# Optimization experiments

Hardware: AMD Instinct MI355X
Metric: run time of the kernel (lower is better)

## Reference

```python
import jax, jax.numpy as jnp
import numpy as np

HIDDEN = 256


def setup_inputs() -> dict:
    key = jax.random.key(0)
    ks = jax.random.split(key, 6)
    b, c_len, q_len, h = 32, 1024, 128, HIDDEN
    # Xavier-uniform bounds for the learned weights
    lim_vec = float(np.sqrt(6.0 / (h + 1)))      # (h, 1) weights
    lim_cq = float(np.sqrt(6.0 / (1 + h)))       # (1, 1, h) weight
    return {
        "context": jax.random.normal(ks[0], (b, c_len, h), dtype=jnp.float32),
        "query": jax.random.normal(ks[1], (b, q_len, h), dtype=jnp.float32),
        "c_mask": jnp.zeros((b, c_len), dtype=bool),
        "q_mask": jnp.zeros((b, q_len), dtype=bool),
        "c_weight": jax.random.uniform(ks[2], (h, 1), jnp.float32, -lim_vec, lim_vec),
        "q_weight": jax.random.uniform(ks[3], (h, 1), jnp.float32, -lim_vec, lim_vec),
        "cq_weight": jax.random.uniform(ks[4], (1, 1, h), jnp.float32, -lim_cq, lim_cq),
        "bias": jnp.zeros((1,), dtype=jnp.float32),
    }


def reference(context, query, c_mask, q_mask, c_weight, q_weight, cq_weight, bias):
    # Trilinear similarity: S[b,i,j] = c_i.w_c + q_j.w_q + (c_i * w_cq).q_j + bias
    s0 = context @ c_weight                                  # (b, c, 1)
    s1 = jnp.swapaxes(query @ q_weight, 1, 2)                # (b, 1, q)
    s2 = jnp.einsum('bch,bqh->bcq', context * cq_weight, query)
    S = s0 + s1 + s2 + bias                                  # (b, c, q)

    S_bar = jax.nn.softmax(S, axis=1)       # softmax over context axis
    S_bar_bar = jax.nn.softmax(S, axis=2)   # softmax over query axis

    A = jnp.einsum('bcq,bqh->bch', S, query)  # note: raw S, as in source
    B = jnp.einsum('bcq,bkq,bkh->bch', S_bar, S_bar_bar, context)

    return jnp.concatenate([context, A, context * A, context * B], axis=2)
```

## Files before the change

kernel.cpp:

```cpp
#include <hip/hip_runtime.h>
#include <cstdint>
#include <cstddef>

#define BATCH 32
#define CLEN  1024
#define QLEN  128
#define HID   256

typedef __attribute__((ext_vector_type(8))) short bf16x8;
typedef __attribute__((ext_vector_type(4))) float f32x4;

#define MFMA(a, b, c) __builtin_amdgcn_mfma_f32_16x16x32_bf16((a), (b), (c), 0, 0, 0)

__device__ __forceinline__ ushort f2b(float f) {
    union { float f; uint u; } v; v.f = f;
    uint r = (v.u + 0x7fffu + ((v.u >> 16) & 1u)) >> 16;
    return (ushort)r;
}
__device__ __forceinline__ float b2f(ushort u) {
    union { uint u; float f; } v; v.u = ((uint)u) << 16;
    return v.f;
}

__global__ __launch_bounds__(256) void prep_ctx_kernel(
    const float* __restrict__ context, const float* __restrict__ cw,
    ushort* __restrict__ ctxT, float* __restrict__ cdot)
{
    __shared__ ushort lds[64][258];
    int bid = blockIdx.x;
    int b = bid >> 4, c0 = (bid & 15) * 64;
    int t = threadIdx.x;
    int r = t >> 2, qd = t & 3;
    const float* src = context + ((size_t)(b * CLEN + c0 + r)) * HID;
    float dot = 0.f;
    #pragma unroll
    for (int j = 0; j < 16; j++) {
        int h = j * 16 + qd * 4;
        float4 v = *reinterpret_cast<const float4*>(src + h);
        float4 w = *reinterpret_cast<const float4*>(cw + h);
        dot += v.x * w.x + v.y * w.y + v.z * w.z + v.w * w.w;
        uint p0 = (uint)f2b(v.x) | ((uint)f2b(v.y) << 16);
        uint p1 = (uint)f2b(v.z) | ((uint)f2b(v.w) << 16);
        *reinterpret_cast<uint*>(&lds[r][h])     = p0;
        *reinterpret_cast<uint*>(&lds[r][h + 2]) = p1;
    }
    dot += __shfl_xor(dot, 1);
    dot += __shfl_xor(dot, 2);
    if (qd == 0) cdot[b * CLEN + c0 + r] = dot;
    __syncthreads();
    ushort* dst = ctxT + ((size_t)(b * HID + t)) * CLEN + c0;
    #pragma unroll
    for (int j = 0; j < 8; j++) {
        uint4 w;
        w.x = (uint)lds[j*8+0][t] | ((uint)lds[j*8+1][t] << 16);
        w.y = (uint)lds[j*8+2][t] | ((uint)lds[j*8+3][t] << 16);
        w.z = (uint)lds[j*8+4][t] | ((uint)lds[j*8+5][t] << 16);
        w.w = (uint)lds[j*8+6][t] | ((uint)lds[j*8+7][t] << 16);
        *reinterpret_cast<uint4*>(dst + j * 8) = w;
    }
}

__global__ __launch_bounds__(256) void prep_q_kernel(
    const float* __restrict__ query, const float* __restrict__ qw,
    ushort* __restrict__ qB, ushort* __restrict__ qT, float* __restrict__ qdot)
{
    __shared__ ushort lds[64][258];
    int bid = blockIdx.x;
    int b = bid >> 1, q0 = (bid & 1) * 64;
    int t = threadIdx.x;
    int r = t >> 2, qd = t & 3;
    const float* src = query + ((size_t)(b * QLEN + q0 + r)) * HID;
    ushort* qBr = qB + ((size_t)(b * QLEN + q0 + r)) * HID;
    float dot = 0.f;
    #pragma unroll
    for (int j = 0; j < 16; j++) {
        int h = j * 16 + qd * 4;
        float4 v = *reinterpret_cast<const float4*>(src + h);
        float4 w = *reinterpret_cast<const float4*>(qw + h);
        dot += v.x * w.x + v.y * w.y + v.z * w.z + v.w * w.w;
        uint p0 = (uint)f2b(v.x) | ((uint)f2b(v.y) << 16);
        uint p1 = (uint)f2b(v.z) | ((uint)f2b(v.w) << 16);
        *reinterpret_cast<uint*>(&lds[r][h])     = p0;
        *reinterpret_cast<uint*>(&lds[r][h + 2]) = p1;
        uint2 pk; pk.x = p0; pk.y = p1;
        *reinterpret_cast<uint2*>(qBr + h) = pk;
    }
    dot += __shfl_xor(dot, 1);
    dot += __shfl_xor(dot, 2);
    if (qd == 0) qdot[b * QLEN + q0 + r] = dot;
    __syncthreads();
    ushort* dst = qT + ((size_t)(b * HID + t)) * QLEN + q0;
    #pragma unroll
    for (int j = 0; j < 8; j++) {
        uint4 w;
        w.x = (uint)lds[j*8+0][t] | ((uint)lds[j*8+1][t] << 16);
        w.y = (uint)lds[j*8+2][t] | ((uint)lds[j*8+3][t] << 16);
        w.z = (uint)lds[j*8+4][t] | ((uint)lds[j*8+5][t] << 16);
        w.w = (uint)lds[j*8+6][t] | ((uint)lds[j*8+7][t] << 16);
        *reinterpret_cast<uint4*>(dst + j * 8) = w;
    }
}

__global__ __launch_bounds__(256) void s_kernel(
    const float* __restrict__ context, const ushort* __restrict__ qB,
    const float* __restrict__ cqw, const float* __restrict__ cdot,
    const float* __restrict__ qdot, const float* __restrict__ bias,
    ushort* __restrict__ S, ushort* __restrict__ P2T)
{
    __shared__ float ldsS[64][132];
    __shared__ float ldsM[64], ldsR[64];
    int ct = blockIdx.x, b = blockIdx.y;
    int c0 = ct * 64;
    int t = threadIdx.x;
    int w = t >> 6, L = t & 63, g = L >> 4, ln = L & 15;
    int wr = w >> 1, wc = w & 1;

    f32x4 acc[2][4];
    #pragma unroll
    for (int mi = 0; mi < 2; mi++)
        #pragma unroll
        for (int ni = 0; ni < 4; ni++) acc[mi][ni] = (f32x4){0.f, 0.f, 0.f, 0.f};

    const float* ctxB = context + ((size_t)(b * CLEN + c0 + wr * 32)) * HID;
    const ushort* qBb = qB + ((size_t)(b * QLEN + wc * 64)) * HID;

    #pragma unroll 2
    for (int kk = 0; kk < 8; kk++) {
        int k = kk * 32 + g * 8;
        float4 w0 = *reinterpret_cast<const float4*>(cqw + k);
        float4 w1 = *reinterpret_cast<const float4*>(cqw + k + 4);
        bf16x8 a[2];
        #pragma unroll
        for (int mi = 0; mi < 2; mi++) {
            const float* p = ctxB + (size_t)(mi * 16 + ln) * HID + k;
            float4 v0 = *reinterpret_cast<const float4*>(p);
            float4 v1 = *reinterpret_cast<const float4*>(p + 4);
            bf16x8 av;
            av[0] = (short)f2b(v0.x * w0.x); av[1] = (short)f2b(v0.y * w0.y);
            av[2] = (short)f2b(v0.z * w0.z); av[3] = (short)f2b(v0.w * w0.w);
            av[4] = (short)f2b(v1.x * w1.x); av[5] = (short)f2b(v1.y * w1.y);
            av[6] = (short)f2b(v1.z * w1.z); av[7] = (short)f2b(v1.w * w1.w);
            a[mi] = av;
        }
        bf16x8 bq[4];
        #pragma unroll
        for (int ni = 0; ni < 4; ni++)
            bq[ni] = *reinterpret_cast<const bf16x8*>(qBb + (size_t)(ni * 16 + ln) * HID + k);
        #pragma unroll
        for (int mi = 0; mi < 2; mi++)
            #pragma unroll
            for (int ni = 0; ni < 4; ni++)
                acc[mi][ni] = MFMA(a[mi], bq[ni], acc[mi][ni]);
    }

    float bv = bias[0];
    float qdv[4];
    #pragma unroll
    for (int ni = 0; ni < 4; ni++) qdv[ni] = qdot[b * QLEN + wc * 64 + ni * 16 + ln];
    #pragma unroll
    for (int mi = 0; mi < 2; mi++)
        #pragma unroll
        for (int r = 0; r < 4; r++) {
            int row = wr * 32 + mi * 16 + g * 4 + r;
            float cd = cdot[b * CLEN + c0 + row] + bv;
            #pragma unroll
            for (int ni = 0; ni < 4; ni++)
                ldsS[row][wc * 64 + ni * 16 + ln] = acc[mi][ni][r] + cd + qdv[ni];
        }
    __syncthreads();
    {
        int row = t >> 2, qs = (t & 3) * 32;
        float4 vr[8];
        float m = -1e30f;
        #pragma unroll
        for (int j = 0; j < 8; j++) {
            vr[j] = *reinterpret_cast<const float4*>(&ldsS[row][qs + j * 4]);
            m = fmaxf(m, fmaxf(fmaxf(vr[j].x, vr[j].y), fmaxf(vr[j].z, vr[j].w)));
        }
        m = fmaxf(m, __shfl_xor(m, 1));
        m = fmaxf(m, __shfl_xor(m, 2));
        float s = 0.f;
        #pragma unroll
        for (int j = 0; j < 8; j++)
            s += __expf(vr[j].x - m) + __expf(vr[j].y - m) +
                 __expf(vr[j].z - m) + __expf(vr[j].w - m);
        s += __shfl_xor(s, 1);
        s += __shfl_xor(s, 2);
        if ((t & 3) == 0) { ldsM[row] = m; ldsR[row] = 1.0f / s; }
    }
    __syncthreads();
    {
        const size_t Sbase = ((size_t)b * CLEN + c0) * QLEN;
        #pragma unroll
        for (int i = 0; i < 8; i++) {
            int flat = t + 256 * i;
            int q4 = flat & 31, c = flat >> 5;
            float4 v = *reinterpret_cast<const float4*>(&ldsS[c][q4 * 4]);
            uint2 pk;
            pk.x = (uint)f2b(v.x) | ((uint)f2b(v.y) << 16);
            pk.y = (uint)f2b(v.z) | ((uint)f2b(v.w) << 16);
            *reinterpret_cast<uint2*>(&S[Sbase + (size_t)c * QLEN + q4 * 4]) = pk;
        }
    }
    {
        int q = t >> 1, half = t & 1;
        ushort* dst = P2T + ((size_t)b * QLEN + q) * CLEN + c0 + half * 32;
        #pragma unroll
        for (int jo = 0; jo < 4; jo++) {
            uint pk[4];
            #pragma unroll
            for (int l = 0; l < 4; l++) {
                int c0l = half * 32 + jo * 8 + l * 2;
                float p0 = __expf(ldsS[c0l][q]     - ldsM[c0l])     * ldsR[c0l];
                float p1 = __expf(ldsS[c0l + 1][q] - ldsM[c0l + 1]) * ldsR[c0l + 1];
                pk[l] = (uint)f2b(p0) | ((uint)f2b(p1) << 16);
            }
            uint4 wv; wv.x = pk[0]; wv.y = pk[1]; wv.z = pk[2]; wv.w = pk[3];
            *reinterpret_cast<uint4*>(dst + jo * 8) = wv;
        }
    }
}

__global__ __launch_bounds__(256) void colstats1_kernel(
    const ushort* __restrict__ S, float* __restrict__ pmax, float* __restrict__ psum)
{
    int b = blockIdx.x, chunk = blockIdx.y;
    int t = threadIdx.x;
    int q = t & 127, half = t >> 7;
    const ushort* Sb = S + ((size_t)b * CLEN + chunk * 128) * QLEN;
    float m = -1e30f, s = 0.f;
    for (int k = 0; k < 64; k++) {
        int c = half + 2 * k;
        float v = b2f(Sb[(size_t)c * QLEN + q]);
        float nm = fmaxf(m, v);
        s = s * __expf(m - nm) + __expf(v - nm);
        m = nm;
    }
    __shared__ float sm[256], ss[256];
    sm[t] = m; ss[t] = s;
    __syncthreads();
    if (t < 128) {
        float m2 = sm[t + 128], s2 = ss[t + 128];
        float M = fmaxf(m, m2);
        float Sv = s * __expf(m - M) + s2 * __expf(m2 - M);
        pmax[((size_t)b * 8 + chunk) * QLEN + q] = M;
        psum[((size_t)b * 8 + chunk) * QLEN + q] = Sv;
    }
}

__global__ __launch_bounds__(256) void colstats2_kernel(
    const float* __restrict__ pmax, const float* __restrict__ psum,
    float* __restrict__ colmax, float* __restrict__ colsumr)
{
    int gid = blockIdx.x * 256 + threadIdx.x;
    int b = gid >> 7, q = gid & 127;
    float m = -1e30f, s = 0.f;
    #pragma unroll
    for (int ch = 0; ch < 8; ch++) {
        float m2 = pmax[((size_t)b * 8 + ch) * QLEN + q];
        float s2 = psum[((size_t)b * 8 + ch) * QLEN + q];
        float M = fmaxf(m, m2);
        s = s * __expf(m - M) + s2 * __expf(m2 - M);
        m = M;
    }
    colmax[gid] = m;
    colsumr[gid] = 1.0f / s;
}

__global__ __launch_bounds__(256) void t_kernel(
    const ushort* __restrict__ ctxT, const ushort* __restrict__ P2T,
    float* __restrict__ Tpart)
{
    int x = blockIdx.x, b = blockIdx.y;
    int h0 = (x >> 2) * 64, ks = x & 3;
    int t = threadIdx.x;
    int w = t >> 6, L = t & 63, g = L >> 4, ln = L & 15;
    int wr = w >> 1, wc = w & 1;

    f32x4 acc[2][4];
    #pragma unroll
    for (int mi = 0; mi < 2; mi++)
        #pragma unroll
        for (int ni = 0; ni < 4; ni++) acc[mi][ni] = (f32x4){0.f, 0.f, 0.f, 0.f};

    const ushort* aB = ctxT + ((size_t)(b * HID + h0 + wr * 32)) * CLEN + ks * 256;
    const ushort* bB = P2T + ((size_t)(b * QLEN + wc * 64)) * CLEN + ks * 256;

    #pragma unroll 2
    for (int kk = 0; kk < 8; kk++) {
        int k = kk * 32 + g * 8;
        bf16x8 a[2], bq[4];
        #pragma unroll
        for (int mi = 0; mi < 2; mi++)
            a[mi] = *reinterpret_cast<const bf16x8*>(aB + (size_t)(mi * 16 + ln) * CLEN + k);
        #pragma unroll
        for (int ni = 0; ni < 4; ni++)
            bq[ni] = *reinterpret_cast<const bf16x8*>(bB + (size_t)(ni * 16 + ln) * CLEN + k);
        #pragma unroll
        for (int mi = 0; mi < 2; mi++)
            #pragma unroll
            for (int ni = 0; ni < 4; ni++)
                acc[mi][ni] = MFMA(a[mi], bq[ni], acc[mi][ni]);
    }
    float* dst = Tpart + (size_t)ks * (BATCH * HID * QLEN);
    #pragma unroll
    for (int mi = 0; mi < 2; mi++)
        #pragma unroll
        for (int ni = 0; ni < 4; ni++)
            #pragma unroll
            for (int r = 0; r < 4; r++) {
                int h = h0 + wr * 32 + mi * 16 + g * 4 + r;
                int q = wc * 64 + ni * 16 + ln;
                dst[((size_t)b * HID + h) * QLEN + q] = acc[mi][ni][r];
            }
}

__global__ __launch_bounds__(256) void t_reduce_kernel(
    const float* __restrict__ Tpart, ushort* __restrict__ Tt)
{
    int gid = blockIdx.x * 256 + threadIdx.x;
    const float4* p = reinterpret_cast<const float4*>(Tpart);
    float4 a = p[gid];
    float4 b = p[gid + 262144];
    float4 c = p[gid + 524288];
    float4 d = p[gid + 786432];
    float4 r = make_float4(a.x + b.x + c.x + d.x, a.y + b.y + c.y + d.y,
                           a.z + b.z + c.z + d.z, a.w + b.w + c.w + d.w);
    uint2 pk;
    pk.x = (uint)f2b(r.x) | ((uint)f2b(r.y) << 16);
    pk.y = (uint)f2b(r.z) | ((uint)f2b(r.w) << 16);
    *reinterpret_cast<uint2*>(Tt + (size_t)gid * 4) = pk;
}

__global__ __launch_bounds__(256) void ab_out_kernel(
    const ushort* __restrict__ S, const ushort* __restrict__ qT,
    const ushort* __restrict__ Tt, const float* __restrict__ context,
    const float* __restrict__ colmax, const float* __restrict__ colsumr,
    float* __restrict__ out)
{
    __shared__ float ldsT[128][68];
    int x = blockIdx.x, b = blockIdx.y;
    int c0 = (x >> 2) * 128, h0 = (x & 3) * 64;
    int t = threadIdx.x;
    int w = t >> 6, L = t & 63, g = L >> 4, ln = L & 15;
    int wr = w >> 1, wc = w & 1;

    f32x4 accA[4][2], accB[4][2];
    #pragma unroll
    for (int mi = 0; mi < 4; mi++)
        #pragma unroll
        for (int ni = 0; ni < 2; ni++) {
            accA[mi][ni] = (f32x4){0.f, 0.f, 0.f, 0.f};
            accB[mi][ni] = (f32x4){0.f, 0.f, 0.f, 0.f};
        }

    const ushort* Srow = S + ((size_t)(b * CLEN + c0 + wr * 64)) * QLEN;
    const ushort* qTb  = qT + ((size_t)(b * HID + h0 + wc * 32)) * QLEN;
    const ushort* TtB  = Tt + ((size_t)(b * HID + h0 + wc * 32)) * QLEN;
    const float* cmB = colmax + b * QLEN;
    const float* crB = colsumr + b * QLEN;

    #pragma unroll
    for (int kk = 0; kk < 4; kk++) {
        int k = kk * 32 + g * 8;
        float4 cm0 = *reinterpret_cast<const float4*>(cmB + k);
        float4 cm1 = *reinterpret_cast<const float4*>(cmB + k + 4);
        float4 cr0 = *reinterpret_cast<const float4*>(crB + k);
        float4 cr1 = *reinterpret_cast<const float4*>(crB + k + 4);
        float cmv[8] = {cm0.x, cm0.y, cm0.z, cm0.w, cm1.x, cm1.y, cm1.z, cm1.w};
        float crv[8] = {cr0.x, cr0.y, cr0.z, cr0.w, cr1.x, cr1.y, cr1.z, cr1.w};
        bf16x8 sa[4], pa[4];
        #pragma unroll
        for (int mi = 0; mi < 4; mi++) {
            sa[mi] = *reinterpret_cast<const bf16x8*>(Srow + (size_t)(mi * 16 + ln) * QLEN + k);
            bf16x8 pv;
            #pragma unroll
            for (int i = 0; i < 8; i++) {
                float f = b2f((ushort)sa[mi][i]);
                pv[i] = (short)f2b(__expf(f - cmv[i]) * crv[i]);
            }
            pa[mi] = pv;
        }
        bf16x8 bq[2], bt[2];
        #pragma unroll
        for (int ni = 0; ni < 2; ni++) {
            bq[ni] = *reinterpret_cast<const bf16x8*>(qTb + (size_t)(ni * 16 + ln) * QLEN + k);
            bt[ni] = *reinterpret_cast<const bf16x8*>(TtB + (size_t)(ni * 16 + ln) * QLEN + k);
        }
        #pragma unroll
        for (int mi = 0; mi < 4; mi++)
            #pragma unroll
            for (int ni = 0; ni < 2; ni++) {
                accA[mi][ni] = MFMA(sa[mi], bq[ni], accA[mi][ni]);
                accB[mi][ni] = MFMA(pa[mi], bt[ni], accB[mi][ni]);
            }
    }

    #pragma unroll
    for (int mi = 0; mi < 4; mi++)
        #pragma unroll
        for (int ni = 0; ni < 2; ni++)
            #pragma unroll
            for (int r = 0; r < 4; r++)
                ldsT[wr * 64 + mi * 16 + g * 4 + r][wc * 32 + ni * 16 + ln] = accA[mi][ni][r];
    __syncthreads();
    #pragma unroll
    for (int i = 0; i < 8; i++) {
        int flat = t + 256 * i;
        int h4 = flat & 15, c = flat >> 4;
        float4 av = *reinterpret_cast<const float4*>(&ldsT[c][h4 * 4]);
        float4 cv = *reinterpret_cast<const float4*>(
            context + ((size_t)(b * CLEN + c0 + c)) * HID + h0 + h4 * 4);
        size_t o = ((size_t)(b * CLEN + c0 + c)) * 1024 + h0 + h4 * 4;
        *reinterpret_cast<float4*>(&out[o]) = cv;
        *reinterpret_cast<float4*>(&out[o + 256]) = av;
        *reinterpret_cast<float4*>(&out[o + 512]) =
            make_float4(cv.x * av.x, cv.y * av.y, cv.z * av.z, cv.w * av.w);
    }
    __syncthreads();
    #pragma unroll
    for (int mi = 0; mi < 4; mi++)
        #pragma unroll
        for (int ni = 0; ni < 2; ni++)
            #pragma unroll
            for (int r = 0; r < 4; r++)
                ldsT[wr * 64 + mi * 16 + g * 4 + r][wc * 32 + ni * 16 + ln] = accB[mi][ni][r];
    __syncthreads();
    #pragma unroll
    for (int i = 0; i < 8; i++) {
        int flat = t + 256 * i;
        int h4 = flat & 15, c = flat >> 4;
        float4 bvv = *reinterpret_cast<const float4*>(&ldsT[c][h4 * 4]);
        float4 cv = *reinterpret_cast<const float4*>(
            context + ((size_t)(b * CLEN + c0 + c)) * HID + h0 + h4 * 4);
        size_t o = ((size_t)(b * CLEN + c0 + c)) * 1024 + h0 + h4 * 4;
        *reinterpret_cast<float4*>(&out[o + 768]) =
            make_float4(cv.x * bvv.x, cv.y * bvv.y, cv.z * bvv.z, cv.w * bvv.w);
    }
}

extern "C" void kernel_launch(void* const* d_in, const int* in_sizes, int n_in,
                              void* d_out, int out_size, void* d_ws, size_t ws_size,
                              hipStream_t stream)
{
    (void)in_sizes; (void)n_in; (void)out_size; (void)ws_size;
    const float* context   = (const float*)d_in[0];
    const float* query     = (const float*)d_in[1];
    const float* c_weight  = (const float*)d_in[4];
    const float* q_weight  = (const float*)d_in[5];
    const float* cq_weight = (const float*)d_in[6];
    const float* bias      = (const float*)d_in[7];
    float* out = (float*)d_out;
    float* wsf = (float*)d_ws;

    ushort* ctxT = (ushort*)(wsf);
    ushort* qB   = (ushort*)(wsf + 4194304);
    ushort* qT   = (ushort*)(wsf + 4718592);
    ushort* S    = (ushort*)(wsf + 5242880);
    ushort* P2T  = (ushort*)(wsf + 7340032);
    ushort* Tt   = (ushort*)(wsf + 9437184);
    float* Tpart   = wsf + 9961472;
    float* cdot    = wsf + 14155776;
    float* qdot    = cdot + 32768;
    float* pmax    = qdot + 4096;
    float* psum    = pmax + 32768;
    float* colmax  = psum + 32768;
    float* colsumr = colmax + 4096;

    prep_ctx_kernel<<<512, 256, 0, stream>>>(context, c_weight, ctxT, cdot);
    prep_q_kernel<<<64, 256, 0, stream>>>(query, q_weight, qB, qT, qdot);
    s_kernel<<<dim3(16, 32), 256, 0, stream>>>(context, qB, cq_weight, cdot, qdot,
                                               bias, S, P2T);
    colstats1_kernel<<<dim3(32, 8), 256, 0, stream>>>(S, pmax, psum);
    colstats2_kernel<<<16, 256, 0, stream>>>(pmax, psum, colmax, colsumr);
    t_kernel<<<dim3(16, 32), 256, 0, stream>>>(ctxT, P2T, Tpart);
    t_reduce_kernel<<<1024, 256, 0, stream>>>(Tpart, Tt);
    ab_out_kernel<<<dim3(32, 32), 256, 0, stream>>>(S, qT, Tt, context,
                                                    colmax, colsumr, out);
}
```

Before: 119.1 us.

## Merge prep kernels, precompute scaled context, single-pass colstats, halve T split-K

Fuses the context and query prep kernels into one launch, and has prep also write a bf16 copy of context scaled by cq_weight. The S kernel can then load bf16 operands directly instead of converting fp32 per tile. The two-stage column-statistics kernels become one two-pass (max then sum) kernel over S, and the T GEMM split-K drops from 4 to 2, which halves the partial-sum traffic in the reduction. This removes launches and redundant conversion work, at the cost of an extra 16 MB bf16 buffer write and fewer blocks in the T kernel.

```diff
diff --git a/kernel.cpp b/kernel.cpp
--- a/kernel.cpp
+++ b/kernel.cpp
@@ -22,89 +22,93 @@
     return v.f;
 }
 
-__global__ __launch_bounds__(256) void prep_ctx_kernel(
-    const float* __restrict__ context, const float* __restrict__ cw,
-    ushort* __restrict__ ctxT, float* __restrict__ cdot)
+__global__ __launch_bounds__(256) void prep_kernel(
+    const float* __restrict__ context, const float* __restrict__ query,
+    const float* __restrict__ cw, const float* __restrict__ qw,
+    const float* __restrict__ cqw,
+    ushort* __restrict__ ctxT, ushort* __restrict__ mcB,
+    ushort* __restrict__ qB, ushort* __restrict__ qT,
+    float* __restrict__ cdot, float* __restrict__ qdot)
 {
     __shared__ ushort lds[64][258];
     int bid = blockIdx.x;
-    int b = bid >> 4, c0 = (bid & 15) * 64;
     int t = threadIdx.x;
     int r = t >> 2, qd = t & 3;
-    const float* src = context + ((size_t)(b * CLEN + c0 + r)) * HID;
-    float dot = 0.f;
-    #pragma unroll
-    for (int j = 0; j < 16; j++) {
-        int h = j * 16 + qd * 4;
-        float4 v = *reinterpret_cast<const float4*>(src + h);
-        float4 w = *reinterpret_cast<const float4*>(cw + h);
-        dot += v.x * w.x + v.y * w.y + v.z * w.z + v.w * w.w;
-        uint p0 = (uint)f2b(v.x) | ((uint)f2b(v.y) << 16);
-        uint p1 = (uint)f2b(v.z) | ((uint)f2b(v.w) << 16);
-        *reinterpret_cast<uint*>(&lds[r][h])     = p0;
-        *reinterpret_cast<uint*>(&lds[r][h + 2]) = p1;
-    }
-    dot += __shfl_xor(dot, 1);
-    dot += __shfl_xor(dot, 2);
-    if (qd == 0) cdot[b * CLEN + c0 + r] = dot;
-    __syncthreads();
-    ushort* dst = ctxT + ((size_t)(b * HID + t)) * CLEN + c0;
-    #pragma unroll
-    for (int j = 0; j < 8; j++) {
-        uint4 w;
-        w.x = (uint)lds[j*8+0][t] | ((uint)lds[j*8+1][t] << 16);
-        w.y = (uint)lds[j*8+2][t] | ((uint)lds[j*8+3][t] << 16);
-        w.z = (uint)lds[j*8+4][t] | ((uint)lds[j*8+5][t] << 16);
-        w.w = (uint)lds[j*8+6][t] | ((uint)lds[j*8+7][t] << 16);
-        *reinterpret_cast<uint4*>(dst + j * 8) = w;
-    }
-}
-
-__global__ __launch_bounds__(256) void prep_q_kernel(
-    const float* __restrict__ query, const float* __restrict__ qw,
-    ushort* __restrict__ qB, ushort* __restrict__ qT, float* __restrict__ qdot)
-{
-    __shared__ ushort lds[64][258];
-    int bid = blockIdx.x;
-    int b = bid >> 1, q0 = (bid & 1) * 64;
-    int t = threadIdx.x;
-    int r = t >> 2, qd = t & 3;
-    const float* src = query + ((size_t)(b * QLEN + q0 + r)) * HID;
-    ushort* qBr = qB + ((size_t)(b * QLEN + q0 + r)) * HID;
-    float dot = 0.f;
-    #pragma unroll
-    for (int j = 0; j < 16; j++) {
-        int h = j * 16 + qd * 4;
-        float4 v = *reinterpret_cast<const float4*>(src + h);
-        float4 w = *reinterpret_cast<const float4*>(qw + h);
-        dot += v.x * w.x + v.y * w.y + v.z * w.z + v.w * w.w;
-        uint p0 = (uint)f2b(v.x) | ((uint)f2b(v.y) << 16);
-        uint p1 = (uint)f2b(v.z) | ((uint)f2b(v.w) << 16);
-        *reinterpret_cast<uint*>(&lds[r][h])     = p0;
-        *reinterpret_cast<uint*>(&lds[r][h + 2]) = p1;
-        uint2 pk; pk.x = p0; pk.y = p1;
-        *reinterpret_cast<uint2*>(qBr + h) = pk;
-    }
-    dot += __shfl_xor(dot, 1);
-    dot += __shfl_xor(dot, 2);
-    if (qd == 0) qdot[b * QLEN + q0 + r] = dot;
-    __syncthreads();
-    ushort* dst = qT + ((size_t)(b * HID + t)) * QLEN + q0;
-    #pragma unroll
-    for (int j = 0; j < 8; j++) {
-        uint4 w;
-        w.x = (uint)lds[j*8+0][t] | ((uint)lds[j*8+1][t] << 16);
-        w.y = (uint)lds[j*8+2][t] | ((uint)lds[j*8+3][t] << 16);
-        w.z = (uint)lds[j*8+4][t] | ((uint)lds[j*8+5][t] << 16);
-        w.w = (uint)lds[j*8+6][t] | ((uint)lds[j*8+7][t] << 16);
-        *reinterpret_cast<uint4*>(dst + j * 8) = w;
+    if (bid < 512) {
+        int b = bid >> 4, c0 = (bid & 15) * 64;
+        const float* src = context + ((size_t)(b * CLEN + c0 + r)) * HID;
+        ushort* mcr = mcB + ((size_t)(b * CLEN + c0 + r)) * HID;
+        float dot = 0.f;
+        #pragma unroll
+        for (int j = 0; j < 16; j++) {
+            int h = j * 16 + qd * 4;
+            float4 v  = *reinterpret_cast<const float4*>(src + h);
+            float4 w  = *reinterpret_cast<const float4*>(cw + h);
+            float4 wc = *reinterpret_cast<const float4*>(cqw + h);
+            dot += v.x * w.x + v.y * w.y + v.z * w.z + v.w * w.w;
+            uint p0 = (uint)f2b(v.x) | ((uint)f2b(v.y) << 16);
+            uint p1 = (uint)f2b(v.z) | ((uint)f2b(v.w) << 16);
+            *reinterpret_cast<uint*>(&lds[r][h])     = p0;
+            *reinterpret_cast<uint*>(&lds[r][h + 2]) = p1;
+            uint2 mc;
+            mc.x = (uint)f2b(v.x * wc.x) | ((uint)f2b(v.y * wc.y) << 16);
+            mc.y = (uint)f2b(v.z * wc.z) | ((uint)f2b(v.w * wc.w) << 16);
+            *reinterpret_cast<uint2*>(mcr + h) = mc;
+        }
+        dot += __shfl_xor(dot, 1);
+        dot += __shfl_xor(dot, 2);
+        if (qd == 0) cdot[b * CLEN + c0 + r] = dot;
+        __syncthreads();
+        ushort* dst = ctxT + ((size_t)(b * HID + t)) * CLEN + c0;
+        #pragma unroll
+        for (int j = 0; j < 8; j++) {
+            uint4 w;
+            w.x = (uint)lds[j*8+0][t] | ((uint)lds[j*8+1][t] << 16);
+            w.y = (uint)lds[j*8+2][t] | ((uint)lds[j*8+3][t] << 16);
+            w.z = (uint)lds[j*8+4][t] | ((uint)lds[j*8+5][t] << 16);
+            w.w = (uint)lds[j*8+6][t] | ((uint)lds[j*8+7][t] << 16);
+            *reinterpret_cast<uint4*>(dst + j * 8) = w;
+        }
+    } else {
+        int bb = bid - 512;
+        int b = bb >> 1, q0 = (bb & 1) * 64;
+        const float* src = query + ((size_t)(b * QLEN + q0 + r)) * HID;
+        ushort* qBr = qB + ((size_t)(b * QLEN + q0 + r)) * HID;
+        float dot = 0.f;
+        #pragma unroll
+        for (int j = 0; j < 16; j++) {
+            int h = j * 16 + qd * 4;
+            float4 v = *reinterpret_cast<const float4*>(src + h);
+            float4 w = *reinterpret_cast<const float4*>(qw + h);
+            dot += v.x * w.x + v.y * w.y + v.z * w.z + v.w * w.w;
+            uint p0 = (uint)f2b(v.x) | ((uint)f2b(v.y) << 16);
+            uint p1 = (uint)f2b(v.z) | ((uint)f2b(v.w) << 16);
+            *reinterpret_cast<uint*>(&lds[r][h])     = p0;
+            *reinterpret_cast<uint*>(&lds[r][h + 2]) = p1;
+            uint2 pk; pk.x = p0; pk.y = p1;
+            *reinterpret_cast<uint2*>(qBr + h) = pk;
+        }
+        dot += __shfl_xor(dot, 1);
+        dot += __shfl_xor(dot, 2);
+        if (qd == 0) qdot[b * QLEN + q0 + r] = dot;
+        __syncthreads();
+        ushort* dst = qT + ((size_t)(b * HID + t)) * QLEN + q0;
+        #pragma unroll
+        for (int j = 0; j < 8; j++) {
+            uint4 w;
+            w.x = (uint)lds[j*8+0][t] | ((uint)lds[j*8+1][t] << 16);
+            w.y = (uint)lds[j*8+2][t] | ((uint)lds[j*8+3][t] << 16);
+            w.z = (uint)lds[j*8+4][t] | ((uint)lds[j*8+5][t] << 16);
+            w.w = (uint)lds[j*8+6][t] | ((uint)lds[j*8+7][t] << 16);
+            *reinterpret_cast<uint4*>(dst + j * 8) = w;
+        }
     }
 }
 
 __global__ __launch_bounds__(256) void s_kernel(
-    const float* __restrict__ context, const ushort* __restrict__ qB,
-    const float* __restrict__ cqw, const float* __restrict__ cdot,
-    const float* __restrict__ qdot, const float* __restrict__ bias,
+    const ushort* __restrict__ mcB, const ushort* __restrict__ qB,
+    const float* __restrict__ cdot, const float* __restrict__ qdot,
+    const float* __restrict__ bias,
     ushort* __restrict__ S, ushort* __restrict__ P2T)
 {
     __shared__ float ldsS[64][132];
@@ -121,28 +125,16 @@
         #pragma unroll
         for (int ni = 0; ni < 4; ni++) acc[mi][ni] = (f32x4){0.f, 0.f, 0.f, 0.f};
 
-    const float* ctxB = context + ((size_t)(b * CLEN + c0 + wr * 32)) * HID;
-    const ushort* qBb = qB + ((size_t)(b * QLEN + wc * 64)) * HID;
+    const ushort* aBase = mcB + ((size_t)(b * CLEN + c0 + wr * 32)) * HID;
+    const ushort* qBb   = qB + ((size_t)(b * QLEN + wc * 64)) * HID;
 
     #pragma unroll 2
     for (int kk = 0; kk < 8; kk++) {
         int k = kk * 32 + g * 8;
-        float4 w0 = *reinterpret_cast<const float4*>(cqw + k);
-        float4 w1 = *reinterpret_cast<const float4*>(cqw + k + 4);
-        bf16x8 a[2];
-        #pragma unroll
-        for (int mi = 0; mi < 2; mi++) {
-            const float* p = ctxB + (size_t)(mi * 16 + ln) * HID + k;
-            float4 v0 = *reinterpret_cast<const float4*>(p);
-            float4 v1 = *reinterpret_cast<const float4*>(p + 4);
-            bf16x8 av;
-            av[0] = (short)f2b(v0.x * w0.x); av[1] = (short)f2b(v0.y * w0.y);
-            av[2] = (short)f2b(v0.z * w0.z); av[3] = (short)f2b(v0.w * w0.w);
-            av[4] = (short)f2b(v1.x * w1.x); av[5] = (short)f2b(v1.y * w1.y);
-            av[6] = (short)f2b(v1.z * w1.z); av[7] = (short)f2b(v1.w * w1.w);
-            a[mi] = av;
-        }
-        bf16x8 bq[4];
+        bf16x8 a[2], bq[4];
+        #pragma unroll
+        for (int mi = 0; mi < 2; mi++)
+            a[mi] = *reinterpret_cast<const bf16x8*>(aBase + (size_t)(mi * 16 + ln) * HID + k);
         #pragma unroll
         for (int ni = 0; ni < 4; ni++)
             bq[ni] = *reinterpret_cast<const bf16x8*>(qBb + (size_t)(ni * 16 + ln) * HID + k);
@@ -221,50 +213,50 @@
     }
 }
 
-__global__ __launch_bounds__(256) void colstats1_kernel(
-    const ushort* __restrict__ S, float* __restrict__ pmax, float* __restrict__ psum)
-{
-    int b = blockIdx.x, chunk = blockIdx.y;
-    int t = threadIdx.x;
-    int q = t & 127, half = t >> 7;
-    const ushort* Sb = S + ((size_t)b * CLEN + chunk * 128) * QLEN;
-    float m = -1e30f, s = 0.f;
-    for (int k = 0; k < 64; k++) {
-        int c = half + 2 * k;
-        float v = b2f(Sb[(size_t)c * QLEN + q]);
-        float nm = fmaxf(m, v);
-        s = s * __expf(m - nm) + __expf(v - nm);
-        m = nm;
-    }
-    __shared__ float sm[256], ss[256];
-    sm[t] = m; ss[t] = s;
-    __syncthreads();
-    if (t < 128) {
-        float m2 = sm[t + 128], s2 = ss[t + 128];
-        float M = fmaxf(m, m2);
-        float Sv = s * __expf(m - M) + s2 * __expf(m2 - M);
-        pmax[((size_t)b * 8 + chunk) * QLEN + q] = M;
-        psum[((size_t)b * 8 + chunk) * QLEN + q] = Sv;
-    }
-}
-
-__global__ __launch_bounds__(256) void colstats2_kernel(
-    const float* __restrict__ pmax, const float* __restrict__ psum,
-    float* __restrict__ colmax, float* __restrict__ colsumr)
-{
-    int gid = blockIdx.x * 256 + threadIdx.x;
-    int b = gid >> 7, q = gid & 127;
-    float m = -1e30f, s = 0.f;
-    #pragma unroll
-    for (int ch = 0; ch < 8; ch++) {
-        float m2 = pmax[((size_t)b * 8 + ch) * QLEN + q];
-        float s2 = psum[((size_t)b * 8 + ch) * QLEN + q];
-        float M = fmaxf(m, m2);
-        s = s * __expf(m - M) + s2 * __expf(m2 - M);
-        m = M;
-    }
-    colmax[gid] = m;
-    colsumr[gid] = 1.0f / s;
+__global__ __launch_bounds__(256) void colstats_kernel(
+    const ushort* __restrict__ S, float* __restrict__ colmax, float* __restrict__ colsumr)
+{
+    __shared__ float red[8][32];
+    __shared__ float Mv[32];
+    int q0 = blockIdx.x * 32, b = blockIdx.y;
+    int t = threadIdx.x, q = t & 31, cs = t >> 5;
+    const ushort* p = S + (size_t)b * CLEN * QLEN + (size_t)cs * 128 * QLEN + q0 + q;
+    float m0 = -1e30f, m1 = -1e30f, m2 = -1e30f, m3 = -1e30f;
+    #pragma unroll 8
+    for (int i = 0; i < 128; i += 4) {
+        m0 = fmaxf(m0, b2f(p[(size_t)(i + 0) * QLEN]));
+        m1 = fmaxf(m1, b2f(p[(size_t)(i + 1) * QLEN]));
+        m2 = fmaxf(m2, b2f(p[(size_t)(i + 2) * QLEN]));
+        m3 = fmaxf(m3, b2f(p[(size_t)(i + 3) * QLEN]));
+    }
+    red[cs][q] = fmaxf(fmaxf(m0, m1), fmaxf(m2, m3));
+    __syncthreads();
+    if (t < 32) {
+        float mm = red[0][t];
+        #pragma unroll
+        for (int j = 1; j < 8; j++) mm = fmaxf(mm, red[j][t]);
+        Mv[t] = mm;
+    }
+    __syncthreads();
+    float M = Mv[q];
+    float s0 = 0.f, s1 = 0.f, s2 = 0.f, s3 = 0.f;
+    #pragma unroll 8
+    for (int i = 0; i < 128; i += 4) {
+        s0 += __expf(b2f(p[(size_t)(i + 0) * QLEN]) - M);
+        s1 += __expf(b2f(p[(size_t)(i + 1) * QLEN]) - M);
+        s2 += __expf(b2f(p[(size_t)(i + 2) * QLEN]) - M);
+        s3 += __expf(b2f(p[(size_t)(i + 3) * QLEN]) - M);
+    }
+    __syncthreads();
+    red[cs][q] = (s0 + s1) + (s2 + s3);
+    __syncthreads();
+    if (t < 32) {
+        float ss = 0.f;
+        #pragma unroll
+        for (int j = 0; j < 8; j++) ss += red[j][t];
+        colmax[b * QLEN + q0 + t]  = Mv[t];
+        colsumr[b * QLEN + q0 + t] = 1.0f / ss;
+    }
 }
 
 __global__ __launch_bounds__(256) void t_kernel(
@@ -272,7 +264,7 @@
     float* __restrict__ Tpart)
 {
     int x = blockIdx.x, b = blockIdx.y;
-    int h0 = (x >> 2) * 64, ks = x & 3;
+    int h0 = (x >> 1) * 64, ks = x & 1;
     int t = threadIdx.x;
     int w = t >> 6, L = t & 63, g = L >> 4, ln = L & 15;
     int wr = w >> 1, wc = w & 1;
@@ -283,11 +275,11 @@
         #pragma unroll
         for (int ni = 0; ni < 4; ni++) acc[mi][ni] = (f32x4){0.f, 0.f, 0.f, 0.f};
 
-    const ushort* aB = ctxT + ((size_t)(b * HID + h0 + wr * 32)) * CLEN + ks * 256;
-    const ushort* bB = P2T + ((size_t)(b * QLEN + wc * 64)) * CLEN + ks * 256;
+    const ushort* aB = ctxT + ((size_t)(b * HID + h0 + wr * 32)) * CLEN + ks * 512;
+    const ushort* bB = P2T + ((size_t)(b * QLEN + wc * 64)) * CLEN + ks * 512;
 
     #pragma unroll 2
-    for (int kk = 0; kk < 8; kk++) {
+    for (int kk = 0; kk < 16; kk++) {
         int k = kk * 32 + g * 8;
         bf16x8 a[2], bq[4];
         #pragma unroll
@@ -322,10 +314,7 @@
     const float4* p = reinterpret_cast<const float4*>(Tpart);
     float4 a = p[gid];
     float4 b = p[gid + 262144];
-    float4 c = p[gid + 524288];
-    float4 d = p[gid + 786432];
-    float4 r = make_float4(a.x + b.x + c.x + d.x, a.y + b.y + c.y + d.y,
-                           a.z + b.z + c.z + d.z, a.w + b.w + c.w + d.w);
+    float4 r = make_float4(a.x + b.x, a.y + b.y, a.z + b.z, a.w + b.w);
     uint2 pk;
     pk.x = (uint)f2b(r.x) | ((uint)f2b(r.y) << 16);
     pk.y = (uint)f2b(r.z) | ((uint)f2b(r.w) << 16);
@@ -451,29 +440,26 @@
     const float* cq_weight = (const float*)d_in[6];
     const float* bias      = (const float*)d_in[7];
     float* out = (float*)d_out;
-    float* wsf = (float*)d_ws;
-
-    ushort* ctxT = (ushort*)(wsf);
-    ushort* qB   = (ushort*)(wsf + 4194304);
-    ushort* qT   = (ushort*)(wsf + 4718592);
-    ushort* S    = (ushort*)(wsf + 5242880);
-    ushort* P2T  = (ushort*)(wsf + 7340032);
-    ushort* Tt   = (ushort*)(wsf + 9437184);
-    float* Tpart   = wsf + 9961472;
-    float* cdot    = wsf + 14155776;
-    float* qdot    = cdot + 32768;
-    float* pmax    = qdot + 4096;
-    float* psum    = pmax + 32768;
-    float* colmax  = psum + 32768;
-    float* colsumr = colmax + 4096;
-
-    prep_ctx_kernel<<<512, 256, 0, stream>>>(context, c_weight, ctxT, cdot);
-    prep_q_kernel<<<64, 256, 0, stream>>>(query, q_weight, qB, qT, qdot);
-    s_kernel<<<dim3(16, 32), 256, 0, stream>>>(context, qB, cq_weight, cdot, qdot,
-                                               bias, S, P2T);
-    colstats1_kernel<<<dim3(32, 8), 256, 0, stream>>>(S, pmax, psum);
-    colstats2_kernel<<<16, 256, 0, stream>>>(pmax, psum, colmax, colsumr);
-    t_kernel<<<dim3(16, 32), 256, 0, stream>>>(ctxT, P2T, Tpart);
+    char* wsb  = (char*)d_ws;
+
+    ushort* ctxT = (ushort*)(wsb);
+    ushort* mcB  = (ushort*)(wsb + 16777216);
+    ushort* qB   = (ushort*)(wsb + 33554432);
+    ushort* qT   = (ushort*)(wsb + 35651584);
+    ushort* S    = (ushort*)(wsb + 37748736);
+    ushort* P2T  = (ushort*)(wsb + 46137344);
+    ushort* Tt   = (ushort*)(wsb + 54525952);
+    float*  Tpart = (float*)(wsb + 56623104);
+    float*  cdot  = (float*)(wsb + 65011712);
+    float*  qdot  = cdot + 32768;
+    float*  colmax  = qdot + 4096;
+    float*  colsumr = colmax + 4096;
+
+    prep_kernel<<<576, 256, 0, stream>>>(context, query, c_weight, q_weight,
+                                         cq_weight, ctxT, mcB, qB, qT, cdot, qdot);
+    s_kernel<<<dim3(16, 32), 256, 0, stream>>>(mcB, qB, cdot, qdot, bias, S, P2T);
+    colstats_kernel<<<dim3(4, 32), 256, 0, stream>>>(S, colmax, colsumr);
+    t_kernel<<<dim3(8, 32), 256, 0, stream>>>(ctxT, P2T, Tpart);
     t_reduce_kernel<<<1024, 256, 0, stream>>>(Tpart, Tt);
     ab_out_kernel<<<dim3(32, 32), 256, 0, stream>>>(S, qT, Tt, context,
                                                     colmax, colsumr, out);
```

Result: faster. 111.8 us (-6.1%).
